# Optimization experiments

Hardware: AMD Instinct MI355X
Metric: run time of the kernel (lower is better)

## Reference

```python
import jax, jax.numpy as jnp
import numpy as np

BATCH = 262144
N_STEPS = 10  # hard-coded `range(10)` in the original get_cycles


def _euler_to_matrix(e):
    # Standard extrinsic xyz convention: R = Rz(z) @ Ry(y) @ Rx(x)
    x, y, z = e[..., 0], e[..., 1], e[..., 2]
    cx, sx = jnp.cos(x), jnp.sin(x)
    cy, sy = jnp.cos(y), jnp.sin(y)
    cz, sz = jnp.cos(z), jnp.sin(z)
    r0 = jnp.stack([cz * cy, cz * sy * sx - sz * cx, cz * sy * cx + sz * sx], -1)
    r1 = jnp.stack([sz * cy, sz * sy * sx + cz * cx, sz * sy * cx - cz * sx], -1)
    r2 = jnp.stack([-sy, cy * sx, cy * cx], -1)
    return jnp.stack([r0, r1, r2], -2)  # (..., 3, 3)


def _matrix_to_euler(R):
    # Classic rotationMatrixToEulerAngles (inverse of Rz@Ry@Rx), with singular branch
    sy = jnp.sqrt(R[..., 0, 0] ** 2 + R[..., 1, 0] ** 2)
    singular = sy < 1e-6
    x = jnp.where(singular,
                  jnp.arctan2(-R[..., 1, 2], R[..., 1, 1]),
                  jnp.arctan2(R[..., 2, 1], R[..., 2, 2]))
    y = jnp.arctan2(-R[..., 2, 0], sy)
    z = jnp.where(singular, jnp.zeros_like(sy), jnp.arctan2(R[..., 1, 0], R[..., 0, 0]))
    return jnp.stack([x, y, z], -1)


def _get_cycles(x):
    # x: (B, 6*N_STEPS), interleaved [t(3), r(3)] per step (per the original reshape())
    x = jax.lax.stop_gradient(x)  # mirrors .detach().numpy() in the original
    g = x.reshape(x.shape[0], N_STEPS, 6)
    t = g[:, :, :3]   # (B, S, 3) translations
    r = g[:, :, 3:]   # (B, S, 3) euler rotations

    # --- translation part ---
    # The original aliases path_pred[0] onto t[0:3] via .numpy() and mutates it
    # in-place across cycle iterations (j=0 doubles it). The resulting recorded
    # values obey: v_0 = t_0 ; v_i = 2*v_{i-1} + sum_{j=1}^{i-1} t_j
    C = jnp.cumsum(t[:, 1:, :], axis=1)  # C[:, k-1, :] = sum_{j=1..k} t_j
    v = [t[:, 0, :]]
    for i in range(1, N_STEPS):
        tail = C[:, i - 2, :] if i >= 2 else jnp.zeros_like(v[0])
        v.append(2.0 * v[-1] + tail)
    trans = jnp.stack(v, axis=1)  # (B, S, 3)

    # --- rotation part ---
    # numpy `*=` is ELEMENTWISE, so cycle i records
    # matrix_to_euler( R(r_1) * prod_{j<i} R(r_j) )  (Hadamard product)
    R = _euler_to_matrix(r)                    # (B, S, 3, 3)
    CP = jnp.cumprod(R, axis=1)                # CP[:, k] = elemwise prod_{j<=k} R_j
    P = jnp.concatenate([jnp.ones_like(R[:, :1]), CP[:, :-1]], axis=1)  # prod_{j<i}
    M = R[:, 1:2] * P                          # (B, S, 3, 3)
    rot = _matrix_to_euler(M)                  # (B, S, 3)

    return jnp.stack([trans, rot], axis=2)     # (B, S, 2, 3)


def setup_inputs():
    key = jax.random.key(0)
    k1, k2 = jax.random.split(key)
    pred = jax.random.normal(k1, (BATCH, 6 * N_STEPS), dtype=jnp.float32)
    gt = jax.random.normal(k2, (BATCH, 6 * N_STEPS), dtype=jnp.float32)
    return {"pred": pred, "gt": gt}


def reference(pred, gt):
    pred_cycles = _get_cycles(pred)
    gt_cycles = _get_cycles(gt)
    loss = jnp.mean((pred_cycles - gt_cycles) ** 2)
    return loss / BATCH  # original divides the MSE by self.batch_size
```

## Files before the change

kernel.cpp:

```cpp
#include <hip/hip_runtime.h>
#include <math.h>

#define NSTEP 10

__device__ __forceinline__ float fast_atan2f(float y, float x) {
    float ax = fabsf(x), ay = fabsf(y);
    float mx = fmaxf(ax, ay);
    float mn = fminf(ax, ay);
    float a = mn * __builtin_amdgcn_rcpf(fmaxf(mx, 1e-38f));
    float s = a * a;
    float r = fmaf(s, fmaf(s, fmaf(s, fmaf(s, 0.0208351f, -0.085133f),
                                   0.180141f), -0.3302995f), 0.9998660f) * a;
    if (ay > ax) r = 1.57079632679f - r;
    if (x < 0.0f) r = 3.14159265359f - r;
    return copysignf(r, y);
}

__device__ __forceinline__ void euler2mat(float x, float y, float z, float R[9]) {
    float sx, cx, sy, cy, sz, cz;
    __sincosf(x, &sx, &cx);
    __sincosf(y, &sy, &cy);
    __sincosf(z, &sz, &cz);
    R[0] = cz * cy; R[1] = cz * sy * sx - sz * cx; R[2] = cz * sy * cx + sz * sx;
    R[3] = sz * cy; R[4] = sz * sy * sx + cz * cx; R[5] = sz * sy * cx - cz * sx;
    R[6] = -sy;     R[7] = cy * sx;                R[8] = cy * cx;
}

__device__ __forceinline__ void emit(float v, float& acc) {
    float d = v - __shfl_xor(v, 1, 64);
    acc = fmaf(d, d, acc);
}

__device__ __forceinline__ void emit_euler(const float M[9], float& acc) {
    float sy = sqrtf(fmaf(M[0], M[0], M[3] * M[3]));
    bool sing = sy < 1e-6f;
    float a0 = sing ? -M[5] : M[7];
    float a1 = sing ?  M[4] : M[8];
    emit(fast_atan2f(a0, a1), acc);
    emit(fast_atan2f(-M[6], sy), acc);
    emit(sing ? 0.0f : fast_atan2f(M[3], M[0]), acc);
}

__global__ __launch_bounds__(256) void cycle_loss_main(
    const float* __restrict__ pred, const float* __restrict__ gt,
    float* __restrict__ partial, int batch)
{
    int gid = blockIdx.x * blockDim.x + threadIdx.x;
    int row = gid >> 1;
    float acc = 0.0f;
    if (row < batch) {
        const float* src = (gid & 1) ? gt : pred;
        const float4* s4 = reinterpret_cast<const float4*>(src + (size_t)row * 60);

        float v[3], cac[3] = {0,0,0}, tprev[3];
        float Q[9];

        float4 A = s4[0], B = s4[1], C = s4[2];
        float4 nA = s4[3], nB = s4[4], nC = s4[5];

        v[0] = A.x; v[1] = A.y; v[2] = A.z;
        emit(v[0], acc); emit(v[1], acc); emit(v[2], acc);
        #pragma unroll
        for (int k = 0; k < 3; ++k) { v[k] *= 2.0f; emit(v[k], acc); }
        tprev[0] = B.z; tprev[1] = B.w; tprev[2] = C.x;

        {
            float R1[9];
            euler2mat(A.w, B.x, B.y, Q);
            euler2mat(C.y, C.z, C.w, R1);
            emit_euler(R1, acc);
            #pragma unroll
            for (int k = 0; k < 9; ++k) Q[k] *= R1[k];
            emit_euler(Q, acc);
            #pragma unroll
            for (int k = 0; k < 9; ++k) Q[k] *= R1[k];
        }

        #pragma unroll 1
        for (int c = 1; c < 5; ++c) {
            A = nA; B = nB; C = nC;
            if (c < 4) { nA = s4[3*c+3]; nB = s4[3*c+4]; nC = s4[3*c+5]; }

            cac[0] += tprev[0]; cac[1] += tprev[1]; cac[2] += tprev[2];
            #pragma unroll
            for (int k = 0; k < 3; ++k) { v[k] = fmaf(2.0f, v[k], cac[k]); emit(v[k], acc); }
            cac[0] += A.x; cac[1] += A.y; cac[2] += A.z;
            #pragma unroll
            for (int k = 0; k < 3; ++k) { v[k] = fmaf(2.0f, v[k], cac[k]); emit(v[k], acc); }
            tprev[0] = B.z; tprev[1] = B.w; tprev[2] = C.x;

            emit_euler(Q, acc);
            {
                float R[9];
                euler2mat(A.w, B.x, B.y, R);
                #pragma unroll
                for (int k = 0; k < 9; ++k) Q[k] *= R[k];
            }
            emit_euler(Q, acc);
            {
                float R[9];
                euler2mat(C.y, C.z, C.w, R);
                #pragma unroll
                for (int k = 0; k < 9; ++k) Q[k] *= R[k];
            }
        }
    }

    int lane = threadIdx.x & 63;
    int wid  = threadIdx.x >> 6;
    #pragma unroll
    for (int off = 32; off > 0; off >>= 1)
        acc += __shfl_down(acc, off, 64);
    __shared__ float warp_s[4];
    if (lane == 0) warp_s[wid] = acc;
    __syncthreads();
    if (threadIdx.x == 0)
        partial[blockIdx.x] = warp_s[0] + warp_s[1] + warp_s[2] + warp_s[3];
}

__global__ __launch_bounds__(256) void cycle_loss_fin(
    const float* __restrict__ partial, float* __restrict__ out,
    int nblocks, float inv)
{
    int t = threadIdx.x;
    float s = 0.0f;
    for (int i = t; i < nblocks; i += 256) s += partial[i];
    int lane = t & 63, wid = t >> 6;
    #pragma unroll
    for (int off = 32; off > 0; off >>= 1)
        s += __shfl_down(s, off, 64);
    __shared__ float warp_s[4];
    if (lane == 0) warp_s[wid] = s;
    __syncthreads();
    if (t == 0)
        out[0] = (warp_s[0] + warp_s[1] + warp_s[2] + warp_s[3]) * inv;
}

extern "C" void kernel_launch(void* const* d_in, const int* in_sizes, int n_in,
                              void* d_out, int out_size, void* d_ws, size_t ws_size,
                              hipStream_t stream) {
    const float* pred = (const float*)d_in[0];
    const float* gt   = (const float*)d_in[1];
    int batch = in_sizes[0] / 60;
    float* partial = (float*)d_ws;

    const int threads = 256;
    const int blocks = (2 * batch + threads - 1) / threads;
    cycle_loss_main<<<blocks, threads, 0, stream>>>(pred, gt, partial, batch);

    double inv = 0.5 / (60.0 * (double)batch * (double)batch);
    cycle_loss_fin<<<1, threads, 0, stream>>>(partial, (float*)d_out, blocks, (float)inv);
}
```

Measured before the change: 155.3 us.

## Stage rows through padded LDS with coalesced loads and use DPP for pair exchange

Each block now loads its 128 pred and 128 gt rows into LDS with fully coalesced scalar loads, padding each row to stride 61 to avoid bank conflicts. Threads then read their row from LDS instead of doing strided per-thread float4 global loads. The pair exchange uses a DPP quad-permute in place of a shuffle, the step loop is fully unrolled, and the unused last rotation multiply is skipped. The cost is about 61KB of LDS per block, which limits occupancy. The batch bound check is dropped, so the kernel assumes batch is a multiple of 128.

```diff
diff --git a/kernel.cpp b/kernel.cpp
--- a/kernel.cpp
+++ b/kernel.cpp
@@ -2,6 +2,9 @@
 #include <math.h>
 
 #define NSTEP 10
+#define ROWS_PER_BLOCK 128
+#define ROW_STRIDE 61
+#define HALF_OFF (ROWS_PER_BLOCK * ROW_STRIDE)
 
 __device__ __forceinline__ float fast_atan2f(float y, float x) {
     float ax = fabsf(x), ay = fabsf(y);
@@ -27,7 +30,8 @@
 }
 
 __device__ __forceinline__ void emit(float v, float& acc) {
-    float d = v - __shfl_xor(v, 1, 64);
+    int pi = __builtin_amdgcn_update_dpp(0, __float_as_int(v), 0xB1, 0xF, 0xF, true);
+    float d = v - __int_as_float(pi);
     acc = fmaf(d, d, acc);
 }
 
@@ -45,29 +49,42 @@
     const float* __restrict__ pred, const float* __restrict__ gt,
     float* __restrict__ partial, int batch)
 {
-    int gid = blockIdx.x * blockDim.x + threadIdx.x;
-    int row = gid >> 1;
+    __shared__ float lds[2 * HALF_OFF];
+    const int tid = threadIdx.x;
+
+    {
+        const size_t gbase = (size_t)blockIdx.x * (ROWS_PER_BLOCK * 60);
+        #pragma unroll
+        for (int it = 0; it < 30; ++it) {
+            int i = tid + it * 256;
+            int lidx = i + i / 60;
+            lds[lidx]            = pred[gbase + i];
+            lds[HALF_OFF + lidx] = gt[gbase + i];
+        }
+    }
+    __syncthreads();
+
     float acc = 0.0f;
-    if (row < batch) {
-        const float* src = (gid & 1) ? gt : pred;
-        const float4* s4 = reinterpret_cast<const float4*>(src + (size_t)row * 60);
+    {
+        const float* row = lds + ((tid & 1) ? HALF_OFF : 0) + (tid >> 1) * ROW_STRIDE;
 
         float v[3], cac[3] = {0,0,0}, tprev[3];
         float Q[9];
 
-        float4 A = s4[0], B = s4[1], C = s4[2];
-        float4 nA = s4[3], nB = s4[4], nC = s4[5];
+        float e0 = row[0], e1 = row[1], e2 = row[2], e3 = row[3];
+        float e4 = row[4], e5 = row[5], e6 = row[6], e7 = row[7];
+        float e8 = row[8], e9 = row[9], e10 = row[10], e11 = row[11];
 
-        v[0] = A.x; v[1] = A.y; v[2] = A.z;
+        v[0] = e0; v[1] = e1; v[2] = e2;
         emit(v[0], acc); emit(v[1], acc); emit(v[2], acc);
         #pragma unroll
         for (int k = 0; k < 3; ++k) { v[k] *= 2.0f; emit(v[k], acc); }
-        tprev[0] = B.z; tprev[1] = B.w; tprev[2] = C.x;
+        tprev[0] = e6; tprev[1] = e7; tprev[2] = e8;
 
         {
             float R1[9];
-            euler2mat(A.w, B.x, B.y, Q);
-            euler2mat(C.y, C.z, C.w, R1);
+            euler2mat(e3, e4, e5, Q);
+            euler2mat(e9, e10, e11, R1);
             emit_euler(R1, acc);
             #pragma unroll
             for (int k = 0; k < 9; ++k) Q[k] *= R1[k];
@@ -76,45 +93,47 @@
             for (int k = 0; k < 9; ++k) Q[k] *= R1[k];
         }
 
-        #pragma unroll 1
+        #pragma unroll
         for (int c = 1; c < 5; ++c) {
-            A = nA; B = nB; C = nC;
-            if (c < 4) { nA = s4[3*c+3]; nB = s4[3*c+4]; nC = s4[3*c+5]; }
+            const float* rc = row + 12 * c;
+            float f0 = rc[0], f1 = rc[1], f2 = rc[2], f3 = rc[3];
+            float f4 = rc[4], f5 = rc[5], f6 = rc[6], f7 = rc[7];
+            float f8 = rc[8], f9 = rc[9], f10 = rc[10], f11 = rc[11];
 
             cac[0] += tprev[0]; cac[1] += tprev[1]; cac[2] += tprev[2];
             #pragma unroll
             for (int k = 0; k < 3; ++k) { v[k] = fmaf(2.0f, v[k], cac[k]); emit(v[k], acc); }
-            cac[0] += A.x; cac[1] += A.y; cac[2] += A.z;
+            cac[0] += f0; cac[1] += f1; cac[2] += f2;
             #pragma unroll
             for (int k = 0; k < 3; ++k) { v[k] = fmaf(2.0f, v[k], cac[k]); emit(v[k], acc); }
-            tprev[0] = B.z; tprev[1] = B.w; tprev[2] = C.x;
+            tprev[0] = f6; tprev[1] = f7; tprev[2] = f8;
 
             emit_euler(Q, acc);
             {
                 float R[9];
-                euler2mat(A.w, B.x, B.y, R);
+                euler2mat(f3, f4, f5, R);
                 #pragma unroll
                 for (int k = 0; k < 9; ++k) Q[k] *= R[k];
             }
             emit_euler(Q, acc);
-            {
+            if (c < 4) {
                 float R[9];
-                euler2mat(C.y, C.z, C.w, R);
+                euler2mat(f9, f10, f11, R);
                 #pragma unroll
                 for (int k = 0; k < 9; ++k) Q[k] *= R[k];
             }
         }
     }
 
-    int lane = threadIdx.x & 63;
-    int wid  = threadIdx.x >> 6;
+    int lane = tid & 63;
+    int wid  = tid >> 6;
     #pragma unroll
     for (int off = 32; off > 0; off >>= 1)
         acc += __shfl_down(acc, off, 64);
     __shared__ float warp_s[4];
     if (lane == 0) warp_s[wid] = acc;
     __syncthreads();
-    if (threadIdx.x == 0)
+    if (tid == 0)
         partial[blockIdx.x] = warp_s[0] + warp_s[1] + warp_s[2] + warp_s[3];
 }
 
@@ -145,7 +164,7 @@
     float* partial = (float*)d_ws;
 
     const int threads = 256;
-    const int blocks = (2 * batch + threads - 1) / threads;
+    const int blocks = batch / ROWS_PER_BLOCK;
     cycle_loss_main<<<blocks, threads, 0, stream>>>(pred, gt, partial, batch);
 
     double inv = 0.5 / (60.0 * (double)batch * (double)batch);
```

Measured after the change: 145.2 us. -6.5%, faster.
